# Kernel optimization log

Measured on AMD Instinct MI355X. Metric: run time of the kernel, lower is better.

Reference implementation:

```python
import jax, jax.numpy as jnp
import numpy as np

N = 4096        # nodes
E = 131072      # edges (avg degree 32)
IN = 512        # in_channels
HID = 512       # hidden_channels
HEADS = 4       # GAT heads
LAYERS = 3      # residual GCN layers
G = 16          # graphs in batch
OUT = 1         # out_channels
NEG_SLOPE = 0.2 # GAT LeakyReLU slope


def setup_inputs() -> dict:
    key = jax.random.key(0)
    ks = jax.random.split(key, 9)
    s = 0.02
    x = jax.random.normal(ks[0], (N, IN), dtype=jnp.float32)
    edge_index = jax.random.randint(ks[1], (2, E), 0, N)
    batch = jnp.sort(jax.random.randint(ks[2], (N,), 0, G))
    W_gat = jax.random.normal(ks[3], (HEADS, IN, HID), dtype=jnp.float32) * s
    a_src = jax.random.normal(ks[4], (HEADS, HID), dtype=jnp.float32) * s
    a_dst = jax.random.normal(ks[5], (HEADS, HID), dtype=jnp.float32) * s
    W_gcn = jax.random.normal(ks[6], (LAYERS, HID, HID), dtype=jnp.float32) * s
    fc_w = jax.random.normal(ks[7], (HID, OUT), dtype=jnp.float32) * s
    fc_b = jnp.zeros((OUT,), dtype=jnp.float32)
    return {"x": x, "edge_index": edge_index, "batch": batch,
            "W_gat": W_gat, "a_src": a_src, "a_dst": a_dst,
            "W_gcn": W_gcn, "fc_w": fc_w, "fc_b": fc_b}


def reference(x, edge_index, batch, W_gat, a_src, a_dst, W_gcn, fc_w, fc_b):
    src, dst = edge_index[0], edge_index[1]

    # ---- LatentRelationCapturerGAT: multi-head GAT, one output per head ----
    h = jnp.einsum('nc,hcd->nhd', x, W_gat)                    # [N,H,D]
    lg_src = jnp.einsum('nhd,hd->nh', h, a_src)                # [N,H]
    lg_dst = jnp.einsum('nhd,hd->nh', h, a_dst)                # [N,H]
    e = jax.nn.leaky_relu(lg_src[src] + lg_dst[dst], NEG_SLOPE)  # [E,H]
    # segment softmax over incoming edges of each destination node
    m = jax.ops.segment_max(e, dst, num_segments=N)            # [N,H]
    w = jnp.exp(e - m[dst])                                    # [E,H]
    z = jax.ops.segment_sum(w, dst, num_segments=N)            # [N,H]
    alpha = w / (z[dst] + 1e-16)                               # [E,H]
    H0 = jax.ops.segment_sum(alpha[:, :, None] * h[src], dst, num_segments=N)  # [N,H,D]

    # ---- dense adjacency build + GCN normalization (shared across heads) ----
    A = jnp.zeros((N, N), dtype=x.dtype).at[src, dst].set(1.0)
    A = A + jnp.eye(N, dtype=x.dtype)                          # self-loops
    dinv = jax.lax.rsqrt(jnp.sum(A, axis=1))                   # deg >= 1
    A_hat = dinv[:, None] * A * dinv[None, :]                  # D^-1/2 (A+I) D^-1/2

    # ---- DeepResidualGCN: H <- relu(A_hat @ H @ W_l) + H (heads batched) ----
    H = H0
    for l in range(W_gcn.shape[0]):
        P = jnp.einsum('nm,mhd->nhd', A_hat, H)                # propagate
        H = jax.nn.relu(jnp.einsum('nhd,de->nhe', P, W_gcn[l])) + H

    # ---- per-head global mean pool, then mean over heads ----
    ones = jnp.ones((N,), dtype=x.dtype)
    cnt = jnp.maximum(jax.ops.segment_sum(ones, batch, num_segments=G), 1.0)  # [G]
    pooled = jax.ops.segment_sum(H, batch, num_segments=G) / cnt[:, None, None]  # [G,H,D]
    feats = pooled.mean(axis=1)                                # [G,D]

    return feats @ fc_w + fc_b                                 # [G,OUT]
```

## Files before the change

kernel.cpp:

```cpp
#include <hip/hip_runtime.h>
#include <cstdint>
#include <cstddef>

#define Nn    4096
#define Ee    131072
#define INC   512
#define HIDC  512
#define HEADS 4
#define NLAY  3
#define GG    16
#define FW    2048

typedef __attribute__((ext_vector_type(8))) short bfrag;
typedef __attribute__((ext_vector_type(4))) float ffrag;

__device__ __forceinline__ ushort f2bf(float v){
  uint u = __builtin_bit_cast(uint, v);
  u += 0x7fffu + ((u>>16)&1u);
  return (ushort)(u>>16);
}
__device__ __forceinline__ float bf2f(ushort s){
  uint u = ((uint)s)<<16; return __builtin_bit_cast(float, u);
}
__device__ __forceinline__ void fma8(float* acc, uint4 g, float w){
  uint u[4] = {g.x, g.y, g.z, g.w};
  #pragma unroll
  for (int q=0;q<4;q++){
    float lo = __builtin_bit_cast(float, u[q]<<16);
    float hi = __builtin_bit_cast(float, u[q] & 0xffff0000u);
    acc[2*q]   += w*lo;
    acc[2*q+1] += w*hi;
  }
}
__device__ __forceinline__ void pack8(void* p, const float* a){
  uint4 o;
  o.x = (uint)f2bf(a[0]) | ((uint)f2bf(a[1])<<16);
  o.y = (uint)f2bf(a[2]) | ((uint)f2bf(a[3])<<16);
  o.z = (uint)f2bf(a[4]) | ((uint)f2bf(a[5])<<16);
  o.w = (uint)f2bf(a[6]) | ((uint)f2bf(a[7])<<16);
  *(uint4*)p = o;
}

__global__ __launch_bounds__(256) void tobf(const float* __restrict__ X, ushort* __restrict__ Xb){
  int i = blockIdx.x*256 + threadIdx.x;
  Xb[i] = f2bf(X[i]);
}

__global__ __launch_bounds__(256) void tbf(const float* __restrict__ W, ushort* __restrict__ T){
  __shared__ float tile[32][33];
  int b = blockIdx.z;
  int r0 = blockIdx.y*32, c0 = blockIdx.x*32;
  int t = threadIdx.x;
  int i = t>>3, j0 = (t&7)*4;
  const float* Wb = W + (size_t)b*512*512;
  float4 v = *(const float4*)(Wb + (size_t)(r0+i)*512 + c0 + j0);
  tile[i][j0]=v.x; tile[i][j0+1]=v.y; tile[i][j0+2]=v.z; tile[i][j0+3]=v.w;
  __syncthreads();
  ushort* o = T + (size_t)b*512*512 + (size_t)(c0+i)*512 + r0 + j0;
  #pragma unroll
  for (int q=0;q<4;q++) o[q] = f2bf(tile[j0+q][i]);
}

__global__ __launch_bounds__(256) void gemm_bf(
    const ushort* __restrict__ A, const ushort* __restrict__ B,
    const ushort* Res, ushort* Cb,
    int M, int N, int K, int relu_res)
{
  __shared__ __align__(16) ushort Ah[2][2048];
  __shared__ __align__(16) ushort Bh[2][4096];
  int t = threadIdx.x;
  int m0 = blockIdx.y*64, n0 = blockIdx.x*128;
  int srA = t>>2, kqA = t&3;
  const ushort* pA = A + (size_t)(m0+srA)*K + kqA*8;
  int wA = (kqA*64 + srA)*8;
  int srB = t>>1, cB = t&1;
  const ushort* pB = B + (size_t)(n0+srB)*K + cB*16;
  int wB0 = ((2*cB)*128 + srB)*8;
  int wB1 = wB0 + 1024;

  int wave = t>>6, lane = t&63;
  int wm = (wave&1)*32, wn = (wave>>1)*64;
  int lm = lane&15, quad = lane>>4;

  ffrag acc[2][4];
  #pragma unroll
  for (int i=0;i<2;i++){
    #pragma unroll
    for (int j=0;j<4;j++) acc[i][j] = (ffrag){0.f,0.f,0.f,0.f};
  }

  uint4 ra  = *(const uint4*)(pA);
  uint4 rb0 = *(const uint4*)(pB);  uint4 rb1 = *(const uint4*)(pB+8);
  *(uint4*)&Ah[0][wA]  = ra;
  *(uint4*)&Bh[0][wB0] = rb0; *(uint4*)&Bh[0][wB1] = rb1;
  if (K > 32){
    ra  = *(const uint4*)(pA+32);
    rb0 = *(const uint4*)(pB+32); rb1 = *(const uint4*)(pB+40);
  }
  __syncthreads();

  for (int k0 = 0; k0 < K; k0 += 32){
    int cur = (k0>>5)&1, nxt = cur^1;
    bfrag af[2];
    #pragma unroll
    for (int mt=0; mt<2; mt++)
      af[mt] = *(const bfrag*)&Ah[cur][(quad*64 + wm + mt*16 + lm)*8];
    #pragma unroll
    for (int nt=0; nt<4; nt++){
      bfrag bf = *(const bfrag*)&Bh[cur][(quad*128 + wn + nt*16 + lm)*8];
      #pragma unroll
      for (int mt=0; mt<2; mt++)
        acc[mt][nt] = __builtin_amdgcn_mfma_f32_16x16x32_bf16(af[mt], bf, acc[mt][nt], 0,0,0);
    }
    if (k0+32 < K){
      *(uint4*)&Ah[nxt][wA]  = ra;
      *(uint4*)&Bh[nxt][wB0] = rb0; *(uint4*)&Bh[nxt][wB1] = rb1;
      if (k0+64 < K){
        ra  = *(const uint4*)(pA+k0+64);
        rb0 = *(const uint4*)(pB+k0+64); rb1 = *(const uint4*)(pB+k0+72);
      }
    }
    __syncthreads();
  }

  #pragma unroll
  for (int mt=0; mt<2; mt++){
    #pragma unroll
    for (int nt=0; nt<4; nt++){
      #pragma unroll
      for (int r=0;r<4;r++){
        int grow = m0 + wm + mt*16 + quad*4 + r;
        int gcol = n0 + wn + nt*16 + lm;
        size_t off = (size_t)grow*N + gcol;
        float v = acc[mt][nt][r];
        if (relu_res) v = fmaxf(v,0.f) + bf2f(Res[off]);
        Cb[off] = f2bf(v);
      }
    }
  }
}

__global__ __launch_bounds__(256) void compute_lg(const ushort* __restrict__ hbf,
    const float* __restrict__ a_src, const float* __restrict__ a_dst,
    float* __restrict__ lgs, float* __restrict__ lgd){
  int n = blockIdx.x; int t = threadIdx.x;
  int hd = t>>6, lane = t&63;
  uint4 g = *(const uint4*)(hbf + (size_t)n*FW + hd*HIDC + lane*8);
  float h[8] = {0,0,0,0,0,0,0,0};
  fma8(h, g, 1.0f);
  float4 as0 = *(const float4*)(a_src + hd*HIDC + lane*8);
  float4 as1 = *(const float4*)(a_src + hd*HIDC + lane*8 + 4);
  float4 ad0 = *(const float4*)(a_dst + hd*HIDC + lane*8);
  float4 ad1 = *(const float4*)(a_dst + hd*HIDC + lane*8 + 4);
  float s1 = h[0]*as0.x + h[1]*as0.y + h[2]*as0.z + h[3]*as0.w
           + h[4]*as1.x + h[5]*as1.y + h[6]*as1.z + h[7]*as1.w;
  float s2 = h[0]*ad0.x + h[1]*ad0.y + h[2]*ad0.z + h[3]*ad0.w
           + h[4]*ad1.x + h[5]*ad1.y + h[6]*ad1.z + h[7]*ad1.w;
  for (int off=32; off; off>>=1){ s1 += __shfl_down(s1,off); s2 += __shfl_down(s2,off); }
  if (lane==0){ lgs[n*HEADS+hd]=s1; lgd[n*HEADS+hd]=s2; }
}

__global__ __launch_bounds__(256) void edge_pass1(const int* __restrict__ src, const int* __restrict__ dst,
    int* __restrict__ indeg, unsigned int* __restrict__ bitmap,
    int* __restrict__ cnt_s, int* __restrict__ flag){
  int e = blockIdx.x*256+threadIdx.x; if (e>=Ee) return;
  int s = src[e], d = dst[e];
  atomicAdd(&indeg[d],1);
  unsigned int key = (unsigned int)s*Nn + (unsigned int)d;
  unsigned int bit = 1u<<(key&31);
  unsigned int old = atomicOr(&bitmap[key>>5], bit);
  int f = (old & bit) ? 0 : 1;
  flag[e] = f;
  if (f) atomicAdd(&cnt_s[s],1);
}

__global__ __launch_bounds__(1024) void exscan2(const int* __restrict__ cnt0, int* __restrict__ rp0,
    const int* __restrict__ cnt1, int* __restrict__ rp1){
  const int* cnt = blockIdx.x ? cnt1 : cnt0;
  int* rowptr    = blockIdx.x ? rp1  : rp0;
  __shared__ int sums[1024];
  int t = threadIdx.x;
  int v[4]; int s=0;
  #pragma unroll
  for (int i=0;i<4;i++){ int idx=t*4+i; v[i] = cnt[idx]; s+=v[i]; }
  sums[t]=s; __syncthreads();
  for (int off=1; off<1024; off<<=1){
    int other = (t>=off)? sums[t-off] : 0;
    __syncthreads();
    sums[t] += other;
    __syncthreads();
  }
  int run = (t>0)? sums[t-1] : 0;
  #pragma unroll
  for (int i=0;i<4;i++){ int idx=t*4+i; rowptr[idx]=run; run+=v[i]; }
  if (t==1023) rowptr[Nn]=sums[1023];
}

__global__ __launch_bounds__(256) void compute_dinv(const int* __restrict__ cnt, float* __restrict__ dinv){
  int n = blockIdx.x*256+threadIdx.x; if (n<Nn) dinv[n] = 1.0f/sqrtf((float)(1+cnt[n]));
}

__global__ __launch_bounds__(256) void edge_pass2(const int* __restrict__ src, const int* __restrict__ dst,
    const int* __restrict__ flag,
    const int* __restrict__ rp_d, int* __restrict__ fill_d, int* __restrict__ slist,
    const int* __restrict__ rp_s, int* __restrict__ fill_s, int2* __restrict__ cw,
    const float* __restrict__ dinv){
  int e = blockIdx.x*256+threadIdx.x; if (e>=Ee) return;
  int s = src[e], d = dst[e];
  int p = atomicAdd(&fill_d[d],1); slist[rp_d[d]+p] = s;
  if (flag[e]){
    int q = atomicAdd(&fill_s[s],1);
    cw[rp_s[s]+q] = make_int2(d, __float_as_int(dinv[d]));
  }
}

__global__ __launch_bounds__(256) void gat_aggregate(const ushort* __restrict__ hbf,
    const float* __restrict__ lgs, const float* __restrict__ lgd,
    const int* __restrict__ rowptr, const int* __restrict__ slist,
    ushort* __restrict__ Hbf){
  int t = threadIdx.x;
  int wv = __builtin_amdgcn_readfirstlane(t>>6);
  int lane = t&63;
  int b = blockIdx.x;
  int hd = __builtin_amdgcn_readfirstlane(b & 3);
  int n = ((b>>2)<<2) + wv;
  int beg = rowptr[n], deg = rowptr[n+1]-beg;
  float ldst = lgd[n*HEADS+hd];
  float m_ = -3.4e38f, z_ = 0.f;
  int   s0 = 0; float v0 = 0.f;
  for (int i=lane; i<deg; i+=64){
    int s = slist[beg+i];
    float v = lgs[s*HEADS+hd] + ldst;
    v = v>0.f ? v : 0.2f*v;
    if (i<64){ s0=s; v0=v; }
    float mn = fmaxf(m_, v);
    z_ = z_*__expf(m_-mn) + __expf(v-mn);
    m_ = mn;
  }
  for (int o=32;o;o>>=1){
    float mo = __shfl_down(m_,o), zo = __shfl_down(z_,o);
    float mn = fmaxf(m_, mo);
    z_ = z_*__expf(m_-mn) + zo*__expf(mo-mn);
    m_ = mn;
  }
  float mx = __shfl(m_,0);
  float zs = __shfl(z_,0);
  float inv = 1.f/(zs+1e-16f);
  float acc[8] = {0,0,0,0,0,0,0,0};
  const ushort* hb = hbf + hd*HIDC + lane*8;
  for (int base=0; base<deg; base+=64){
    float al; int s;
    if (base==0){
      s = s0;
      al = (lane<deg) ? __expf(v0-mx)*inv : 0.f;
    } else {
      int i = base+lane;
      al = 0.f; s = 0;
      if (i<deg){
        s = slist[beg+i];
        float v = lgs[s*HEADS+hd] + ldst; v = v>0.f ? v : 0.2f*v;
        al = __expf(v-mx)*inv;
      }
    }
    int cn = min(64, deg-base);
    int c = 0;
    for (; c+8<=cn; c+=8){
      uint4 g[8]; float a[8];
      #pragma unroll
      for (int q=0;q<8;q++){
        a[q] = __shfl(al,c+q);
        int ss = __shfl(s,c+q);
        g[q] = *(const uint4*)(hb + (size_t)ss*FW);
      }
      #pragma unroll
      for (int q=0;q<8;q++) fma8(acc, g[q], a[q]);
    }
    for (; c+4<=cn; c+=4){
      uint4 g[4]; float a[4];
      #pragma unroll
      for (int q=0;q<4;q++){
        a[q] = __shfl(al,c+q);
        int ss = __shfl(s,c+q);
        g[q] = *(const uint4*)(hb + (size_t)ss*FW);
      }
      #pragma unroll
      for (int q=0;q<4;q++) fma8(acc, g[q], a[q]);
    }
    for (; c<cn; c++){
      float a = __shfl(al,c);
      int ss  = __shfl(s,c);
      uint4 g = *(const uint4*)(hb + (size_t)ss*FW);
      fma8(acc, g, a);
    }
  }
  size_t off = (size_t)n*FW + hd*HIDC + lane*8;
  pack8(Hbf + off, acc);
}

__global__ __launch_bounds__(256) void spmm_bf(const ushort* __restrict__ Hbf,
    ushort* __restrict__ Phi,
    const int* __restrict__ rowptr, const int2* __restrict__ cw, const float* __restrict__ dinv){
  int t = threadIdx.x;
  int wv = __builtin_amdgcn_readfirstlane(t>>6);
  int lane = t&63;
  int b = blockIdx.x;
  int ck = __builtin_amdgcn_readfirstlane(b & 3);
  int n = ((b>>2)<<2) + wv;
  int f = (ck<<9) + lane*8;
  float di = dinv[n];
  float acc[8] = {0,0,0,0,0,0,0,0};
  const ushort* hb = Hbf + f;
  uint4 self = *(const uint4*)(hb + (size_t)n*FW);
  fma8(acc, self, di*di);
  int beg = rowptr[n], end = rowptr[n+1];
  for (int base=beg; base<end; base+=64){
    int i = base + lane;
    int m = n; float w = 0.f;
    if (i < end){ int2 e = cw[i]; m = e.x; w = di*__int_as_float(e.y); }
    int cn = min(64, end-base);
    int c = 0;
    for (; c+8<=cn; c+=8){
      uint4 g[8]; float ww[8];
      #pragma unroll
      for (int q=0;q<8;q++){
        ww[q] = __shfl(w,c+q);
        int mm = __shfl(m,c+q);
        g[q] = *(const uint4*)(hb + (size_t)mm*FW);
      }
      #pragma unroll
      for (int q=0;q<8;q++) fma8(acc, g[q], ww[q]);
    }
    for (; c+4<=cn; c+=4){
      uint4 g[4]; float ww[4];
      #pragma unroll
      for (int q=0;q<4;q++){
        ww[q] = __shfl(w,c+q);
        int mm = __shfl(m,c+q);
        g[q] = *(const uint4*)(hb + (size_t)mm*FW);
      }
      #pragma unroll
      for (int q=0;q<4;q++) fma8(acc, g[q], ww[q]);
    }
    for (; c<cn; c++){
      int mm   = __shfl(m,c);
      float ww = __shfl(w,c);
      uint4 g = *(const uint4*)(hb + (size_t)mm*FW);
      fma8(acc, g, ww);
    }
  }
  pack8(Phi + (size_t)n*FW + f, acc);
}

__global__ __launch_bounds__(256) void graph_offsets(const int* __restrict__ batch, int* __restrict__ goff){
  __shared__ int cnt[GG];
  int t = threadIdx.x;
  if (t<GG) cnt[t]=0;
  __syncthreads();
  for (int i=t;i<Nn;i+=256) atomicAdd(&cnt[batch[i]],1);
  __syncthreads();
  if (t==0){ int run=0; for (int g=0; g<GG; g++){ goff[g]=run; run+=cnt[g]; } goff[GG]=run; }
}
__global__ __launch_bounds__(256) void pool_accum(const ushort* __restrict__ Hb,
    const int* __restrict__ batch, float* __restrict__ psum){
  int d2 = blockIdx.y*256 + threadIdx.x;
  int n0 = blockIdx.x*32;
  int g = batch[n0];
  float s0 = 0.f, s1 = 0.f;
  for (int k=0;k<32;k++){
    int n = n0+k;
    int gn = batch[n];
    if (gn != g){
      atomicAdd(&psum[(size_t)g*FW + d2*2],   s0);
      atomicAdd(&psum[(size_t)g*FW + d2*2+1], s1);
      s0=0.f; s1=0.f; g=gn;
    }
    uint v = *(const uint*)(Hb + (size_t)n*FW + d2*2);
    s0 += bf2f((ushort)(v&0xffff));
    s1 += bf2f((ushort)(v>>16));
  }
  atomicAdd(&psum[(size_t)g*FW + d2*2],   s0);
  atomicAdd(&psum[(size_t)g*FW + d2*2+1], s1);
}
__global__ __launch_bounds__(256) void final_out(const float* __restrict__ psum,
    const int* __restrict__ goff,
    const float* __restrict__ fc_w, const float* __restrict__ fc_b, float* __restrict__ out){
  int g = blockIdx.x; int t = threadIdx.x;
  float cinv = 0.25f / fmaxf((float)(goff[g+1]-goff[g]), 1.f);
  float p = 0.f;
  for (int d=t; d<HIDC; d+=256){
    float f = cinv*(psum[(size_t)g*FW+d] + psum[(size_t)g*FW+HIDC+d]
                  + psum[(size_t)g*FW+2*HIDC+d] + psum[(size_t)g*FW+3*HIDC+d]);
    p += f*fc_w[d];
  }
  __shared__ float red[4];
  for (int off=32; off; off>>=1) p += __shfl_down(p,off);
  if ((t&63)==0) red[t>>6]=p;
  __syncthreads();
  if (t==0) out[g] = red[0]+red[1]+red[2]+red[3] + fc_b[0];
}

extern "C" void kernel_launch(void* const* d_in, const int* in_sizes, int n_in,
                              void* d_out, int out_size, void* d_ws, size_t ws_size,
                              hipStream_t stream){
  const float* x      = (const float*)d_in[0];
  const int*   ei     = (const int*)d_in[1];
  const int*   batch  = (const int*)d_in[2];
  const float* W_gat  = (const float*)d_in[3];
  const float* a_src  = (const float*)d_in[4];
  const float* a_dst  = (const float*)d_in[5];
  const float* W_gcn  = (const float*)d_in[6];
  const float* fc_w   = (const float*)d_in[7];
  const float* fc_b   = (const float*)d_in[8];
  float* out = (float*)d_out;
  const int* src = ei;
  const int* dst = ei + Ee;

  char* w = (char*)d_ws;
  size_t off = 0;
  auto alloc = [&](size_t bytes)->char*{ char* p = w + off; off = (off + bytes + 255) & ~(size_t)255; return p; };
  ushort* hbf    = (ushort*)alloc((size_t)Nn*FW*2);
  ushort* Hbf    = (ushort*)alloc((size_t)Nn*FW*2);
  ushort* Xbf    = (ushort*)alloc((size_t)Nn*INC*2);
  ushort* WgatT  = (ushort*)alloc((size_t)HEADS*INC*HIDC*2);
  ushort* WgcnT  = (ushort*)alloc((size_t)NLAY*HIDC*HIDC*2);
  float* lgs    = (float*)alloc((size_t)Nn*HEADS*4);
  float* lgd    = (float*)alloc((size_t)Nn*HEADS*4);
  int* indeg    = (int*)alloc(Nn*4);
  int* fill_d   = (int*)alloc(Nn*4);
  int* cnt_s    = (int*)alloc(Nn*4);
  int* fill_s   = (int*)alloc(Nn*4);
  float* psum   = (float*)alloc((size_t)GG*FW*4);
  unsigned int* bitmap = (unsigned int*)alloc((size_t)Nn*Nn/8);
  size_t zero_bytes = (size_t)Nn*4*4 + (size_t)GG*FW*4 + (size_t)Nn*Nn/8;
  int* rowptr_d = (int*)alloc((Nn+1)*4);
  int* slist    = (int*)alloc(Ee*4);
  int* rowptr_s = (int*)alloc((Nn+1)*4);
  int2* cwlist  = (int2*)alloc((size_t)Ee*8);
  int* flag     = (int*)alloc(Ee*4);
  float* dinv   = (float*)alloc(Nn*4);
  int* goff     = (int*)alloc((GG+1)*4);
  ushort* Phi   = hbf;

  hipMemsetAsync(indeg, 0, zero_bytes, stream);

  tobf<<<(Nn*INC)/256,256,0,stream>>>(x, Xbf);
  tbf<<<dim3(16,16,HEADS),256,0,stream>>>(W_gat, WgatT);
  tbf<<<dim3(16,16,NLAY),256,0,stream>>>(W_gcn, WgcnT);

  gemm_bf<<<dim3(FW/128, Nn/64),256,0,stream>>>(Xbf, WgatT,
      nullptr, hbf, Nn, FW, INC, 0);
  compute_lg<<<Nn,256,0,stream>>>(hbf, a_src, a_dst, lgs, lgd);

  edge_pass1<<<Ee/256,256,0,stream>>>(src, dst, indeg, bitmap, cnt_s, flag);
  exscan2<<<2,1024,0,stream>>>(indeg, rowptr_d, cnt_s, rowptr_s);
  compute_dinv<<<Nn/256,256,0,stream>>>(cnt_s, dinv);
  edge_pass2<<<Ee/256,256,0,stream>>>(src, dst, flag, rowptr_d, fill_d, slist,
                                      rowptr_s, fill_s, cwlist, dinv);
  gat_aggregate<<<Nn,256,0,stream>>>(hbf, lgs, lgd, rowptr_d, slist, Hbf);

  for (int l=0;l<NLAY;l++){
    spmm_bf<<<Nn,256,0,stream>>>(Hbf, Phi, rowptr_s, cwlist, dinv);
    gemm_bf<<<dim3(HIDC/128, (Nn*HEADS)/64),256,0,stream>>>(Phi,
        WgcnT + (size_t)l*HIDC*HIDC,
        Hbf, Hbf, Nn*HEADS, HIDC, HIDC, 1);
  }

  graph_offsets<<<1,256,0,stream>>>(batch, goff);
  pool_accum<<<dim3(Nn/32, FW/512),256,0,stream>>>(Hbf, batch, psum);
  final_out<<<GG,256,0,stream>>>(psum, goff, fc_w, fc_b, out);
}
```

Before: 379.6 us.

## Merge prep kernels, fold scan/dinv/offsets, and simplify gather loops

Merges the bf16 conversion, the weight transposes and the first edge pass into one launch. It also folds the degree scan, the dinv computation and the graph offsets into a single three-block kernel, which removes several small launches. The GAT aggregation and SpMM loops now read edge indices through wave-uniform (scalar) loads and process edges in unrolled groups of 8, instead of loading them per lane and broadcasting with shuffles. This drops the shuffle overhead, but attention weights are now recomputed per edge (an exp per edge per lane), and the big merged prep kernel mixes unrelated work in one grid.

New measurement: 370.4 us. -2.4%, faster.

```diff
diff --git a/kernel.cpp b/kernel.cpp
--- a/kernel.cpp
+++ b/kernel.cpp
@@ -41,24 +41,43 @@
   *(uint4*)p = o;
 }
 
-__global__ __launch_bounds__(256) void tobf(const float* __restrict__ X, ushort* __restrict__ Xb){
-  int i = blockIdx.x*256 + threadIdx.x;
-  Xb[i] = f2bf(X[i]);
-}
-
-__global__ __launch_bounds__(256) void tbf(const float* __restrict__ W, ushort* __restrict__ T){
+__global__ __launch_bounds__(256) void prep(
+    const float* __restrict__ x, ushort* __restrict__ Xb,
+    const float* __restrict__ Wgat, ushort* __restrict__ Tgat,
+    const float* __restrict__ Wgcn, ushort* __restrict__ Tgcn,
+    const int* __restrict__ src, const int* __restrict__ dst,
+    int* __restrict__ indeg, unsigned int* __restrict__ bitmap,
+    int* __restrict__ cnt_s, int* __restrict__ flag){
   __shared__ float tile[32][33];
-  int b = blockIdx.z;
-  int r0 = blockIdx.y*32, c0 = blockIdx.x*32;
-  int t = threadIdx.x;
-  int i = t>>3, j0 = (t&7)*4;
-  const float* Wb = W + (size_t)b*512*512;
-  float4 v = *(const float4*)(Wb + (size_t)(r0+i)*512 + c0 + j0);
-  tile[i][j0]=v.x; tile[i][j0+1]=v.y; tile[i][j0+2]=v.z; tile[i][j0+3]=v.w;
-  __syncthreads();
-  ushort* o = T + (size_t)b*512*512 + (size_t)(c0+i)*512 + r0 + j0;
-  #pragma unroll
-  for (int q=0;q<4;q++) o[q] = f2bf(tile[j0+q][i]);
+  int b = blockIdx.x, t = threadIdx.x;
+  if (b < 8192){
+    int i = b*256 + t;
+    Xb[i] = f2bf(x[i]);
+  } else if (b < 9984){
+    int idx = b - 8192;
+    int z = idx >> 8, xy = idx & 255;
+    const float* W; ushort* T; int bb;
+    if (z < 4){ W = Wgat; T = Tgat; bb = z; } else { W = Wgcn; T = Tgcn; bb = z-4; }
+    int r0 = (xy>>4)*32, c0 = (xy&15)*32;
+    int i = t>>3, j0 = (t&7)*4;
+    const float* Wb = W + (size_t)bb*512*512;
+    float4 v = *(const float4*)(Wb + (size_t)(r0+i)*512 + c0 + j0);
+    tile[i][j0]=v.x; tile[i][j0+1]=v.y; tile[i][j0+2]=v.z; tile[i][j0+3]=v.w;
+    __syncthreads();
+    ushort* o = T + (size_t)bb*512*512 + (size_t)(c0+i)*512 + r0 + j0;
+    #pragma unroll
+    for (int q=0;q<4;q++) o[q] = f2bf(tile[j0+q][i]);
+  } else {
+    int e = (b-9984)*256 + t; if (e>=Ee) return;
+    int s = src[e], d = dst[e];
+    atomicAdd(&indeg[d],1);
+    unsigned int key = (unsigned int)s*Nn + (unsigned int)d;
+    unsigned int bit = 1u<<(key&31);
+    unsigned int old = atomicOr(&bitmap[key>>5], bit);
+    int f = (old & bit) ? 0 : 1;
+    flag[e] = f;
+    if (f) atomicAdd(&cnt_s[s],1);
+  }
 }
 
 __global__ __launch_bounds__(256) void gemm_bf(
@@ -160,26 +179,22 @@
   if (lane==0){ lgs[n*HEADS+hd]=s1; lgd[n*HEADS+hd]=s2; }
 }
 
-__global__ __launch_bounds__(256) void edge_pass1(const int* __restrict__ src, const int* __restrict__ dst,
-    int* __restrict__ indeg, unsigned int* __restrict__ bitmap,
-    int* __restrict__ cnt_s, int* __restrict__ flag){
-  int e = blockIdx.x*256+threadIdx.x; if (e>=Ee) return;
-  int s = src[e], d = dst[e];
-  atomicAdd(&indeg[d],1);
-  unsigned int key = (unsigned int)s*Nn + (unsigned int)d;
-  unsigned int bit = 1u<<(key&31);
-  unsigned int old = atomicOr(&bitmap[key>>5], bit);
-  int f = (old & bit) ? 0 : 1;
-  flag[e] = f;
-  if (f) atomicAdd(&cnt_s[s],1);
-}
-
-__global__ __launch_bounds__(1024) void exscan2(const int* __restrict__ cnt0, int* __restrict__ rp0,
-    const int* __restrict__ cnt1, int* __restrict__ rp1){
-  const int* cnt = blockIdx.x ? cnt1 : cnt0;
-  int* rowptr    = blockIdx.x ? rp1  : rp0;
+__global__ __launch_bounds__(1024) void scan3(const int* __restrict__ indeg, int* __restrict__ rp_d,
+    const int* __restrict__ cnt_s, int* __restrict__ rp_s, float* __restrict__ dinv,
+    const int* __restrict__ batch, int* __restrict__ goff){
   __shared__ int sums[1024];
+  __shared__ int cnt2[GG];
   int t = threadIdx.x;
+  if (blockIdx.x == 2){
+    if (t<GG) cnt2[t]=0;
+    __syncthreads();
+    for (int i=t;i<Nn;i+=1024) atomicAdd(&cnt2[batch[i]],1);
+    __syncthreads();
+    if (t==0){ int run=0; for (int g=0; g<GG; g++){ goff[g]=run; run+=cnt2[g]; } goff[GG]=run; }
+    return;
+  }
+  const int* cnt = blockIdx.x ? cnt_s : indeg;
+  int* rowptr    = blockIdx.x ? rp_s  : rp_d;
   int v[4]; int s=0;
   #pragma unroll
   for (int i=0;i<4;i++){ int idx=t*4+i; v[i] = cnt[idx]; s+=v[i]; }
@@ -192,12 +207,11 @@
   }
   int run = (t>0)? sums[t-1] : 0;
   #pragma unroll
-  for (int i=0;i<4;i++){ int idx=t*4+i; rowptr[idx]=run; run+=v[i]; }
+  for (int i=0;i<4;i++){
+    int idx=t*4+i; rowptr[idx]=run; run+=v[i];
+    if (blockIdx.x) dinv[idx] = 1.0f/sqrtf((float)(1+v[i]));
+  }
   if (t==1023) rowptr[Nn]=sums[1023];
-}
-
-__global__ __launch_bounds__(256) void compute_dinv(const int* __restrict__ cnt, float* __restrict__ dinv){
-  int n = blockIdx.x*256+threadIdx.x; if (n<Nn) dinv[n] = 1.0f/sqrtf((float)(1+cnt[n]));
 }
 
 __global__ __launch_bounds__(256) void edge_pass2(const int* __restrict__ src, const int* __restrict__ dst,
@@ -224,15 +238,15 @@
   int b = blockIdx.x;
   int hd = __builtin_amdgcn_readfirstlane(b & 3);
   int n = ((b>>2)<<2) + wv;
-  int beg = rowptr[n], deg = rowptr[n+1]-beg;
+  int beg = __builtin_amdgcn_readfirstlane(rowptr[n]);
+  int end = __builtin_amdgcn_readfirstlane(rowptr[n+1]);
+  int deg = end - beg;
   float ldst = lgd[n*HEADS+hd];
   float m_ = -3.4e38f, z_ = 0.f;
-  int   s0 = 0; float v0 = 0.f;
   for (int i=lane; i<deg; i+=64){
     int s = slist[beg+i];
     float v = lgs[s*HEADS+hd] + ldst;
     v = v>0.f ? v : 0.2f*v;
-    if (i<64){ s0=s; v0=v; }
     float mn = fmaxf(m_, v);
     z_ = z_*__expf(m_-mn) + __expf(v-mn);
     m_ = mn;
@@ -248,50 +262,24 @@
   float inv = 1.f/(zs+1e-16f);
   float acc[8] = {0,0,0,0,0,0,0,0};
   const ushort* hb = hbf + hd*HIDC + lane*8;
-  for (int base=0; base<deg; base+=64){
-    float al; int s;
-    if (base==0){
-      s = s0;
-      al = (lane<deg) ? __expf(v0-mx)*inv : 0.f;
-    } else {
-      int i = base+lane;
-      al = 0.f; s = 0;
-      if (i<deg){
-        s = slist[beg+i];
-        float v = lgs[s*HEADS+hd] + ldst; v = v>0.f ? v : 0.2f*v;
-        al = __expf(v-mx)*inv;
-      }
+  int i = beg;
+  for (; i+8<=end; i+=8){
+    int s[8]; uint4 g[8];
+    #pragma unroll
+    for (int q=0;q<8;q++) s[q] = slist[i+q];
+    #pragma unroll
+    for (int q=0;q<8;q++) g[q] = *(const uint4*)(hb + (size_t)s[q]*FW);
+    #pragma unroll
+    for (int q=0;q<8;q++){
+      float v = lgs[s[q]*HEADS+hd] + ldst; v = v>0.f ? v : 0.2f*v;
+      fma8(acc, g[q], __expf(v-mx)*inv);
     }
-    int cn = min(64, deg-base);
-    int c = 0;
-    for (; c+8<=cn; c+=8){
-      uint4 g[8]; float a[8];
-      #pragma unroll
-      for (int q=0;q<8;q++){
-        a[q] = __shfl(al,c+q);
-        int ss = __shfl(s,c+q);
-        g[q] = *(const uint4*)(hb + (size_t)ss*FW);
-      }
-      #pragma unroll
-      for (int q=0;q<8;q++) fma8(acc, g[q], a[q]);
-    }
-    for (; c+4<=cn; c+=4){
-      uint4 g[4]; float a[4];
-      #pragma unroll
-      for (int q=0;q<4;q++){
-        a[q] = __shfl(al,c+q);
-        int ss = __shfl(s,c+q);
-        g[q] = *(const uint4*)(hb + (size_t)ss*FW);
-      }
-      #pragma unroll
-      for (int q=0;q<4;q++) fma8(acc, g[q], a[q]);
-    }
-    for (; c<cn; c++){
-      float a = __shfl(al,c);
-      int ss  = __shfl(s,c);
-      uint4 g = *(const uint4*)(hb + (size_t)ss*FW);
-      fma8(acc, g, a);
-    }
+  }
+  for (; i<end; i++){
+    int s = slist[i];
+    uint4 g = *(const uint4*)(hb + (size_t)s*FW);
+    float v = lgs[s*HEADS+hd] + ldst; v = v>0.f ? v : 0.2f*v;
+    fma8(acc, g, __expf(v-mx)*inv);
   }
   size_t off = (size_t)n*FW + hd*HIDC + lane*8;
   pack8(Hbf + off, acc);
@@ -312,54 +300,26 @@
   const ushort* hb = Hbf + f;
   uint4 self = *(const uint4*)(hb + (size_t)n*FW);
   fma8(acc, self, di*di);
-  int beg = rowptr[n], end = rowptr[n+1];
-  for (int base=beg; base<end; base+=64){
-    int i = base + lane;
-    int m = n; float w = 0.f;
-    if (i < end){ int2 e = cw[i]; m = e.x; w = di*__int_as_float(e.y); }
-    int cn = min(64, end-base);
-    int c = 0;
-    for (; c+8<=cn; c+=8){
-      uint4 g[8]; float ww[8];
-      #pragma unroll
-      for (int q=0;q<8;q++){
-        ww[q] = __shfl(w,c+q);
-        int mm = __shfl(m,c+q);
-        g[q] = *(const uint4*)(hb + (size_t)mm*FW);
-      }
-      #pragma unroll
-      for (int q=0;q<8;q++) fma8(acc, g[q], ww[q]);
-    }
-    for (; c+4<=cn; c+=4){
-      uint4 g[4]; float ww[4];
-      #pragma unroll
-      for (int q=0;q<4;q++){
-        ww[q] = __shfl(w,c+q);
-        int mm = __shfl(m,c+q);
-        g[q] = *(const uint4*)(hb + (size_t)mm*FW);
-      }
-      #pragma unroll
-      for (int q=0;q<4;q++) fma8(acc, g[q], ww[q]);
-    }
-    for (; c<cn; c++){
-      int mm   = __shfl(m,c);
-      float ww = __shfl(w,c);
-      uint4 g = *(const uint4*)(hb + (size_t)mm*FW);
-      fma8(acc, g, ww);
-    }
+  int beg = __builtin_amdgcn_readfirstlane(rowptr[n]);
+  int end = __builtin_amdgcn_readfirstlane(rowptr[n+1]);
+  int i = beg;
+  for (; i+8<=end; i+=8){
+    int2 e[8]; uint4 g[8];
+    #pragma unroll
+    for (int q=0;q<8;q++) e[q] = cw[i+q];
+    #pragma unroll
+    for (int q=0;q<8;q++) g[q] = *(const uint4*)(hb + (size_t)e[q].x*FW);
+    #pragma unroll
+    for (int q=0;q<8;q++) fma8(acc, g[q], di*__int_as_float(e[q].y));
+  }
+  for (; i<end; i++){
+    int2 e = cw[i];
+    uint4 g = *(const uint4*)(hb + (size_t)e.x*FW);
+    fma8(acc, g, di*__int_as_float(e.y));
   }
   pack8(Phi + (size_t)n*FW + f, acc);
 }
 
-__global__ __launch_bounds__(256) void graph_offsets(const int* __restrict__ batch, int* __restrict__ goff){
-  __shared__ int cnt[GG];
-  int t = threadIdx.x;
-  if (t<GG) cnt[t]=0;
-  __syncthreads();
-  for (int i=t;i<Nn;i+=256) atomicAdd(&cnt[batch[i]],1);
-  __syncthreads();
-  if (t==0){ int run=0; for (int g=0; g<GG; g++){ goff[g]=run; run+=cnt[g]; } goff[GG]=run; }
-}
 __global__ __launch_bounds__(256) void pool_accum(const ushort* __restrict__ Hb,
     const int* __restrict__ batch, float* __restrict__ psum){
   int d2 = blockIdx.y*256 + threadIdx.x;
@@ -443,17 +403,14 @@
 
   hipMemsetAsync(indeg, 0, zero_bytes, stream);
 
-  tobf<<<(Nn*INC)/256,256,0,stream>>>(x, Xbf);
-  tbf<<<dim3(16,16,HEADS),256,0,stream>>>(W_gat, WgatT);
-  tbf<<<dim3(16,16,NLAY),256,0,stream>>>(W_gcn, WgcnT);
+  prep<<<10496,256,0,stream>>>(x, Xbf, W_gat, WgatT, W_gcn, WgcnT,
+                               src, dst, indeg, bitmap, cnt_s, flag);
 
   gemm_bf<<<dim3(FW/128, Nn/64),256,0,stream>>>(Xbf, WgatT,
       nullptr, hbf, Nn, FW, INC, 0);
   compute_lg<<<Nn,256,0,stream>>>(hbf, a_src, a_dst, lgs, lgd);
 
-  edge_pass1<<<Ee/256,256,0,stream>>>(src, dst, indeg, bitmap, cnt_s, flag);
-  exscan2<<<2,1024,0,stream>>>(indeg, rowptr_d, cnt_s, rowptr_s);
-  compute_dinv<<<Nn/256,256,0,stream>>>(cnt_s, dinv);
+  scan3<<<3,1024,0,stream>>>(indeg, rowptr_d, cnt_s, rowptr_s, dinv, batch, goff);
   edge_pass2<<<Ee/256,256,0,stream>>>(src, dst, flag, rowptr_d, fill_d, slist,
                                       rowptr_s, fill_s, cwlist, dinv);
   gat_aggregate<<<Nn,256,0,stream>>>(hbf, lgs, lgd, rowptr_d, slist, Hbf);
@@ -465,7 +422,6 @@
         Hbf, Hbf, Nn*HEADS, HIDC, HIDC, 1);
   }
 
-  graph_offsets<<<1,256,0,stream>>>(batch, goff);
   pool_accum<<<dim3(Nn/32, FW/512),256,0,stream>>>(Hbf, batch, psum);
   final_out<<<GG,256,0,stream>>>(psum, goff, fc_w, fc_b, out);
 }
```
